# Performance work log

Hardware: AMD Instinct MI355X
Metric: run time of the kernel (lower is better)

The kernel has to match this reference:

```python
import jax, jax.numpy as jnp
import numpy as np

B = 8
N_ANCHORS = 262144
PROPOSAL_COUNT = 1000
IOU_THRESHOLD = 0.7
SOFT_NMS = True
PERFORMANCE_COUNT = 5000
MEAN = np.array([0.0, 0.0, 0.0, 0.0], np.float32)
STD = np.array([0.1, 0.1, 0.2, 0.2], np.float32)
CLIP_RATIO = 16.0 / 1000.0
SOFT_NMS_SIGMA = 0.5  # tf.image.non_max_suppression_with_scores default used by pad_nms
NEG = jnp.float32(-1e9)


def setup_inputs() -> dict:
    key = jax.random.key(0)
    k1, k2, k3, k4, k5 = jax.random.split(key, 5)
    rpn_score = jax.random.uniform(k1, (B, N_ANCHORS, 1), jnp.float32)  # sigmoid-like objectness
    rpn_regress = jax.random.normal(k2, (B, N_ANCHORS, 4), jnp.float32)
    # anchors in normalized x1,y1,x2,y2; centers in [0,1], sizes in [0.02,0.3] (a few fall outside -> exercises valid path)
    cx = jax.random.uniform(k3, (N_ANCHORS,), jnp.float32)
    cy = jax.random.uniform(k4, (N_ANCHORS,), jnp.float32)
    wh = jax.random.uniform(k5, (N_ANCHORS, 2), jnp.float32, minval=0.02, maxval=0.3)
    anchors = jnp.stack([cx - wh[:, 0] * 0.5, cy - wh[:, 1] * 0.5,
                         cx + wh[:, 0] * 0.5, cy + wh[:, 1] * 0.5], axis=-1)
    return {"rpn_score": rpn_score, "rpn_regress": rpn_regress, "anchors": anchors}


def delta2bbox(anchors, deltas):
    # standard mmdet-style decode: denormalize deltas, clip dw/dh, shift/scale anchor box
    d = deltas * jnp.asarray(STD) + jnp.asarray(MEAN)
    max_ratio = abs(float(np.log(CLIP_RATIO)))
    dxy = d[..., :2]
    dwh = jnp.clip(d[..., 2:], -max_ratio, max_ratio)
    awh = anchors[..., 2:] - anchors[..., :2]          # anchor w,h
    actr = (anchors[..., 2:] + anchors[..., :2]) * 0.5  # anchor cx,cy
    ctr = actr + dxy * awh
    wh = awh * jnp.exp(dwh)
    return jnp.concatenate([ctr - wh * 0.5, ctr + wh * 0.5], axis=-1)  # x1,y1,x2,y2


def nms_single(boxes, scores):
    # greedy (soft-)NMS on [P,4] boxes / [P] scores, emitting PROPOSAL_COUNT boxes (zero-padded).
    # IoU is coordinate-order agnostic, so we stay in x1y1x2y2 (TF code round-trips through y1x1y2x2).
    area = (boxes[:, 2] - boxes[:, 0]) * (boxes[:, 3] - boxes[:, 1])

    def step(scores_c, _):
        i = jnp.argmax(scores_c)
        s = scores_c[i]
        b = boxes[i]
        lt = jnp.maximum(b[:2], boxes[:, :2])
        rb = jnp.minimum(b[2:], boxes[:, 2:])
        inter = jnp.prod(jnp.clip(rb - lt, 0.0, None), axis=-1)
        iou = inter / (area[i] + area - inter + 1e-12)
        if SOFT_NMS:
            new_scores = scores_c * jnp.exp(-0.5 * iou * iou / SOFT_NMS_SIGMA)
        else:
            new_scores = jnp.where(iou > IOU_THRESHOLD, NEG, scores_c)
        new_scores = new_scores.at[i].set(NEG)
        sel = jnp.where(s > NEG * 0.5, b, jnp.zeros_like(b))  # zero-pad once candidates exhausted
        return new_scores, sel

    _, out = jax.lax.scan(step, scores, None, length=PROPOSAL_COUNT)
    return out  # [PROPOSAL_COUNT, 4]


def reference(rpn_score, rpn_regress, anchors):
    score = jnp.squeeze(rpn_score, axis=-1)  # [B, A]
    # valid-anchor filtering: TF gathers valid indices (dynamic shape); equivalently mask scores so
    # invalid anchors never survive top-k (num_valid >> performance_count here).
    valid = ((anchors[:, 2] <= 1) & (anchors[:, 3] <= 1) &
             (anchors[:, 0] >= 0) & (anchors[:, 1] >= 0))
    score = jnp.where(valid[None, :], score, -1.0)

    proposals = delta2bbox(anchors[None], rpn_regress)  # [B, A, 4]

    top_scores, top_idx = jax.lax.top_k(score, PERFORMANCE_COUNT)         # [B, P]
    proposals = jnp.take_along_axis(proposals, top_idx[..., None], axis=1)  # [B, P, 4]
    proposals = jnp.clip(proposals, 0.0, 1.0)

    proposals = jax.vmap(nms_single)(proposals, top_scores)  # [B, PROPOSAL_COUNT, 4] (x1,y1,x2,y2)
    return jax.lax.stop_gradient(proposals)
```

## Files before the change

### kernel.cpp

```cpp
#include <hip/hip_runtime.h>
#include <stdint.h>

#pragma clang fp contract(off)

#define N_ANCH 262144
#define BATCH 8
#define TOPK 5000
#define PROP 1000
#define SORTN 8192
#define NEGF -1000000000.0f
#define MAXR 4.135166556742356f
#define NMS_T 512
#define HBINS 256

__device__ __forceinline__ unsigned ord32(float f){
  unsigned u = __float_as_uint(f);
  return (u & 0x80000000u) ? ~u : (u | 0x80000000u);
}
__device__ __forceinline__ float unord32(unsigned o){
  unsigned u = (o & 0x80000000u) ? (o & 0x7FFFFFFFu) : ~o;
  return __uint_as_float(u);
}

__device__ __forceinline__ float masked_score(const float* __restrict__ score,
                                              const float4* __restrict__ anchors,
                                              int b, int i){
  float4 a = anchors[i];
  bool valid = (a.z <= 1.0f) && (a.w <= 1.0f) && (a.x >= 0.0f) && (a.y >= 0.0f);
  float s = score[(size_t)b*N_ANCH + i];
  return valid ? s : -1.0f;
}

__global__ void k_hist1(const float* __restrict__ score, const float4* __restrict__ anchors,
                        unsigned* __restrict__ hist){
  __shared__ unsigned lh[HBINS];
  int b = blockIdx.y; int t = threadIdx.x;
  lh[t] = 0; __syncthreads();
  int base = blockIdx.x * 8192;
  for (int r = 0; r < 32; ++r){
    int i = base + r*256 + t;
    float s = masked_score(score, anchors, b, i);
    unsigned o = ord32(s);
    if (o >= 0xBF000000u){
      int bin = (int)(o >> 16) - 0xBF00;
      atomicAdd(&lh[bin], 1u);
    }
  }
  __syncthreads();
  unsigned v = lh[t];
  if (v) atomicAdd(&hist[(size_t)b*HBINS + t], v);
}

__global__ void k_find1(const unsigned* __restrict__ hist, unsigned* __restrict__ meta){
  int b = blockIdx.x; int t = threadIdx.x;
  __shared__ unsigned part[HBINS];
  part[t] = hist[(size_t)b*HBINS + t];
  __syncthreads();
  if (t == 0){
    unsigned cum = 0; int bsel = 0;
    for (int bin = 128; bin >= 0; --bin){
      cum += part[bin];
      if (cum >= TOPK){ bsel = bin; break; }
    }
    meta[b*8+2] = ((unsigned)(0xBF00 + bsel)) << 16;
  }
}

__global__ void k_compact(const float* __restrict__ score, const float4* __restrict__ anchors,
                          unsigned* __restrict__ meta, unsigned long long* __restrict__ cand){
  int b = blockIdx.y;
  int i = blockIdx.x*blockDim.x + threadIdx.x;
  float s = masked_score(score, anchors, b, i);
  unsigned o = ord32(s);
  unsigned T = meta[b*8+2];
  if (o >= T){
    unsigned pos = atomicAdd(&meta[b*8+3], 1u);
    if (pos < SORTN) cand[(size_t)b*SORTN + pos] = (((unsigned long long)(~o)) << 32) | (unsigned)i;
  }
}

__global__ void __launch_bounds__(1024) k_sort(const unsigned* __restrict__ meta,
                       const unsigned long long* __restrict__ cand,
                       unsigned long long* __restrict__ sorted){
  __shared__ unsigned long long keys[SORTN];
  int b = blockIdx.x; int t = threadIdx.x;
  unsigned cnt = meta[b*8+3];
  if (cnt > (unsigned)SORTN) cnt = SORTN;
  for (unsigned j = t; j < SORTN; j += 1024u)
    keys[j] = (j < cnt) ? cand[(size_t)b*SORTN + j] : ~0ull;
  __syncthreads();
  for (unsigned k = 2; k <= SORTN; k <<= 1){
    for (unsigned j = k>>1; j > 0; j >>= 1){
      for (unsigned i = t; i < SORTN; i += 1024u){
        unsigned l = i ^ j;
        if (l > i){
          unsigned long long a = keys[i], c = keys[l];
          bool up = ((i & k) == 0u);
          if ((a > c) == up){ keys[i] = c; keys[l] = a; }
        }
      }
      __syncthreads();
    }
  }
  for (unsigned j = t; j < TOPK; j += 1024u) sorted[(size_t)b*TOPK + j] = keys[j];
}

#define NMS_UPD(J, S_) do{                                                   \
  int j_ = (J);                                                              \
  if (it > 0){                                                               \
    if (j_ == prevBest){                                                     \
      S_ = NEGF;                                                             \
    } else {                                                                 \
      float4 B_ = bx4[j_];                                                   \
      float ltx_ = fmaxf(bbx, B_.x);                                         \
      float lty_ = fmaxf(bby, B_.y);                                         \
      float rbx_ = fminf(bbz, B_.z);                                         \
      float rby_ = fminf(bbw, B_.w);                                         \
      float iw_ = fmaxf(rbx_-ltx_, 0.f);                                     \
      float ih_ = fmaxf(rby_-lty_, 0.f);                                     \
      float inter_ = iw_*ih_;                                                \
      float aj_ = (B_.z-B_.x)*(B_.w-B_.y);                                   \
      float iou_ = inter_/(ba + aj_ - inter_ + 1e-12f);                      \
      S_ = S_*expf(-(iou_*iou_));                                            \
    }                                                                        \
  }                                                                          \
  if (S_ > bs){ bs = S_; bp = j_; }                                          \
}while(0)

__global__ void __launch_bounds__(NMS_T) k_nms(const unsigned long long* __restrict__ sorted,
                      const float4* __restrict__ anchors, const float4* __restrict__ regress,
                      float* __restrict__ out){
  __shared__ float4 bx4[TOPK];
  __shared__ float  scin[TOPK];
  __shared__ unsigned long long pk[8];
  int b = blockIdx.x; int t = threadIdx.x;
  for (int j = t; j < TOPK; j += NMS_T){
    unsigned long long key = sorted[(size_t)b*TOPK + j];
    unsigned o = ~(unsigned)(key>>32);
    unsigned idx = (unsigned)key;
    float s = unord32(o);
    float4 a = anchors[idx];
    float4 d = regress[(size_t)b*N_ANCH + idx];
    float dx = d.x*0.1f, dy = d.y*0.1f;
    float dw = d.z*0.2f, dh = d.w*0.2f;
    dw = fminf(fmaxf(dw, -MAXR), MAXR);
    dh = fminf(fmaxf(dh, -MAXR), MAXR);
    float aw = a.z - a.x, ah = a.w - a.y;
    float cx = (a.z + a.x)*0.5f, cy = (a.w + a.y)*0.5f;
    float ncx = cx + dx*aw, ncy = cy + dy*ah;
    float nw = aw*expf(dw), nh = ah*expf(dh);
    float x1 = ncx - nw*0.5f, y1 = ncy - nh*0.5f;
    float x2 = ncx + nw*0.5f, y2 = ncy + nh*0.5f;
    x1 = fminf(fmaxf(x1,0.f),1.f); y1 = fminf(fmaxf(y1,0.f),1.f);
    x2 = fminf(fmaxf(x2,0.f),1.f); y2 = fminf(fmaxf(y2,0.f),1.f);
    bx4[j] = make_float4(x1,y1,x2,y2);
    scin[j] = s;
  }
  __syncthreads();
  float S0 = scin[t + 0*NMS_T];
  float S1 = scin[t + 1*NMS_T];
  float S2 = scin[t + 2*NMS_T];
  float S3 = scin[t + 3*NMS_T];
  float S4 = scin[t + 4*NMS_T];
  float S5 = scin[t + 5*NMS_T];
  float S6 = scin[t + 6*NMS_T];
  float S7 = scin[t + 7*NMS_T];
  float S8 = scin[t + 8*NMS_T];
  float S9 = (t + 9*NMS_T < TOPK) ? scin[t + 9*NMS_T] : -INFINITY;
  int lane = t & 63, wid = t >> 6;
  int prevBest = -1;
  float bbx = 0.f, bby = 0.f, bbz = 0.f, bbw = 0.f;
  float ba = 0.f;
  for (int it = 0; it < PROP; ++it){
    float bs = -INFINITY; int bp = 0;
    NMS_UPD(t + 0*NMS_T, S0);
    NMS_UPD(t + 1*NMS_T, S1);
    NMS_UPD(t + 2*NMS_T, S2);
    NMS_UPD(t + 3*NMS_T, S3);
    NMS_UPD(t + 4*NMS_T, S4);
    NMS_UPD(t + 5*NMS_T, S5);
    NMS_UPD(t + 6*NMS_T, S6);
    NMS_UPD(t + 7*NMS_T, S7);
    NMS_UPD(t + 8*NMS_T, S8);
    if (t + 9*NMS_T < TOPK) NMS_UPD(t + 9*NMS_T, S9);
    unsigned long long key = (((unsigned long long)ord32(bs))<<32) | (unsigned)(0xFFFFFFFFu - (unsigned)bp);
    #pragma unroll
    for (int m = 1; m < 64; m <<= 1){
      unsigned long long k2 = __shfl_xor(key, m);
      if (k2 > key) key = k2;
    }
    if (lane == 0) pk[wid] = key;
    __syncthreads();
    #pragma unroll
    for (int w = 0; w < 8; ++w){
      unsigned long long k2 = pk[w];
      if (k2 > key) key = k2;
    }
    int p = (int)(0xFFFFFFFFu - (unsigned)key);
    prevBest = p;
    float4 bbv = bx4[p];
    bbx = bbv.x; bby = bbv.y; bbz = bbv.z; bbw = bbv.w;
    ba = (bbz-bbx)*(bbw-bby);
    if (t == 0){
      float s = unord32((unsigned)(key>>32));
      float4 ob = (s > NEGF*0.5f) ? bbv : make_float4(0.f,0.f,0.f,0.f);
      *(float4*)(out + ((size_t)b*PROP + it)*4) = ob;
    }
    __syncthreads();
  }
}

extern "C" void kernel_launch(void* const* d_in, const int* in_sizes, int n_in,
                              void* d_out, int out_size, void* d_ws, size_t ws_size,
                              hipStream_t stream){
  const float*  score   = (const float*) d_in[0];
  const float4* regress = (const float4*)d_in[1];
  const float4* anchors = (const float4*)d_in[2];
  float* out = (float*)d_out;
  char* ws = (char*)d_ws;
  unsigned* hist = (unsigned*)(ws + 0);
  unsigned* meta = (unsigned*)(ws + 8192);
  unsigned long long* cand   = (unsigned long long*)(ws + 16384);
  unsigned long long* sorted = (unsigned long long*)(ws + 16384 + 524288);

  hipMemsetAsync(ws, 0, 16384, stream);
  dim3 gh(N_ANCH/8192, BATCH);
  k_hist1<<<gh, 256, 0, stream>>>(score, anchors, hist);
  k_find1<<<BATCH, HBINS, 0, stream>>>(hist, meta);
  dim3 gc(N_ANCH/256, BATCH);
  k_compact<<<gc, 256, 0, stream>>>(score, anchors, meta, cand);
  k_sort<<<BATCH, 1024, 0, stream>>>(meta, cand, sorted);
  k_nms<<<BATCH, NMS_T, 0, stream>>>(sorted, anchors, regress, out);
}
```

Measured before the change: 3.172 ms.

## Keep NMS boxes in registers and double-buffer reduction slots to drop a barrier

Each thread now keeps its ten candidate boxes, areas and scores in registers, so the per-iteration IoU loop no longer reads boxes from LDS. Precomputed areas also remove the per-iteration area computation. The per-wave partial maxima are double-buffered by iteration parity, which removes the second __syncthreads in each of the 1000 serial NMS iterations. The cost is higher register pressure with 512 threads per block, and correctness now depends on the parity buffering to avoid a read-after-write race.

```diff
diff --git a/kernel.cpp b/kernel.cpp
--- a/kernel.cpp
+++ b/kernel.cpp
@@ -11,6 +11,7 @@
 #define NEGF -1000000000.0f
 #define MAXR 4.135166556742356f
 #define NMS_T 512
+#define NMS_K 10
 #define HBINS 256
 
 __device__ __forceinline__ unsigned ord32(float f){
@@ -105,108 +106,98 @@
   for (unsigned j = t; j < TOPK; j += 1024u) sorted[(size_t)b*TOPK + j] = keys[j];
 }
 
-#define NMS_UPD(J, S_) do{                                                   \
-  int j_ = (J);                                                              \
-  if (it > 0){                                                               \
-    if (j_ == prevBest){                                                     \
-      S_ = NEGF;                                                             \
-    } else {                                                                 \
-      float4 B_ = bx4[j_];                                                   \
-      float ltx_ = fmaxf(bbx, B_.x);                                         \
-      float lty_ = fmaxf(bby, B_.y);                                         \
-      float rbx_ = fminf(bbz, B_.z);                                         \
-      float rby_ = fminf(bbw, B_.w);                                         \
-      float iw_ = fmaxf(rbx_-ltx_, 0.f);                                     \
-      float ih_ = fmaxf(rby_-lty_, 0.f);                                     \
-      float inter_ = iw_*ih_;                                                \
-      float aj_ = (B_.z-B_.x)*(B_.w-B_.y);                                   \
-      float iou_ = inter_/(ba + aj_ - inter_ + 1e-12f);                      \
-      S_ = S_*expf(-(iou_*iou_));                                            \
-    }                                                                        \
-  }                                                                          \
-  if (S_ > bs){ bs = S_; bp = j_; }                                          \
-}while(0)
-
 __global__ void __launch_bounds__(NMS_T) k_nms(const unsigned long long* __restrict__ sorted,
                       const float4* __restrict__ anchors, const float4* __restrict__ regress,
                       float* __restrict__ out){
   __shared__ float4 bx4[TOPK];
-  __shared__ float  scin[TOPK];
-  __shared__ unsigned long long pk[8];
+  __shared__ unsigned long long pk[2][8];
   int b = blockIdx.x; int t = threadIdx.x;
-  for (int j = t; j < TOPK; j += NMS_T){
-    unsigned long long key = sorted[(size_t)b*TOPK + j];
-    unsigned o = ~(unsigned)(key>>32);
-    unsigned idx = (unsigned)key;
-    float s = unord32(o);
-    float4 a = anchors[idx];
-    float4 d = regress[(size_t)b*N_ANCH + idx];
-    float dx = d.x*0.1f, dy = d.y*0.1f;
-    float dw = d.z*0.2f, dh = d.w*0.2f;
-    dw = fminf(fmaxf(dw, -MAXR), MAXR);
-    dh = fminf(fmaxf(dh, -MAXR), MAXR);
-    float aw = a.z - a.x, ah = a.w - a.y;
-    float cx = (a.z + a.x)*0.5f, cy = (a.w + a.y)*0.5f;
-    float ncx = cx + dx*aw, ncy = cy + dy*ah;
-    float nw = aw*expf(dw), nh = ah*expf(dh);
-    float x1 = ncx - nw*0.5f, y1 = ncy - nh*0.5f;
-    float x2 = ncx + nw*0.5f, y2 = ncy + nh*0.5f;
-    x1 = fminf(fmaxf(x1,0.f),1.f); y1 = fminf(fmaxf(y1,0.f),1.f);
-    x2 = fminf(fmaxf(x2,0.f),1.f); y2 = fminf(fmaxf(y2,0.f),1.f);
-    bx4[j] = make_float4(x1,y1,x2,y2);
-    scin[j] = s;
-  }
-  __syncthreads();
-  float S0 = scin[t + 0*NMS_T];
-  float S1 = scin[t + 1*NMS_T];
-  float S2 = scin[t + 2*NMS_T];
-  float S3 = scin[t + 3*NMS_T];
-  float S4 = scin[t + 4*NMS_T];
-  float S5 = scin[t + 5*NMS_T];
-  float S6 = scin[t + 6*NMS_T];
-  float S7 = scin[t + 7*NMS_T];
-  float S8 = scin[t + 8*NMS_T];
-  float S9 = (t + 9*NMS_T < TOPK) ? scin[t + 9*NMS_T] : -INFINITY;
+  float4 bbx[NMS_K]; float sar[NMS_K]; float sco[NMS_K];
+  #pragma unroll
+  for (int k=0;k<NMS_K;++k){
+    int j = t + k*NMS_T;
+    if (j < TOPK){
+      unsigned long long key = sorted[(size_t)b*TOPK + j];
+      unsigned o = ~(unsigned)(key>>32);
+      unsigned idx = (unsigned)key;
+      float s = unord32(o);
+      float4 a = anchors[idx];
+      float4 d = regress[(size_t)b*N_ANCH + idx];
+      float dx = d.x*0.1f, dy = d.y*0.1f;
+      float dw = d.z*0.2f, dh = d.w*0.2f;
+      dw = fminf(fmaxf(dw, -MAXR), MAXR);
+      dh = fminf(fmaxf(dh, -MAXR), MAXR);
+      float aw = a.z - a.x, ah = a.w - a.y;
+      float cx = (a.z + a.x)*0.5f, cy = (a.w + a.y)*0.5f;
+      float ncx = cx + dx*aw, ncy = cy + dy*ah;
+      float nw = aw*expf(dw), nh = ah*expf(dh);
+      float x1 = ncx - nw*0.5f, y1 = ncy - nh*0.5f;
+      float x2 = ncx + nw*0.5f, y2 = ncy + nh*0.5f;
+      x1 = fminf(fmaxf(x1,0.f),1.f); y1 = fminf(fmaxf(y1,0.f),1.f);
+      x2 = fminf(fmaxf(x2,0.f),1.f); y2 = fminf(fmaxf(y2,0.f),1.f);
+      float4 box = make_float4(x1,y1,x2,y2);
+      bbx[k] = box; bx4[j] = box;
+      sar[k] = (x2-x1)*(y2-y1);
+      sco[k] = s;
+    } else {
+      bbx[k] = make_float4(0.f,0.f,0.f,0.f);
+      sar[k] = 0.f;
+      sco[k] = -INFINITY;
+    }
+  }
+  __syncthreads();
   int lane = t & 63, wid = t >> 6;
   int prevBest = -1;
-  float bbx = 0.f, bby = 0.f, bbz = 0.f, bbw = 0.f;
+  float4 bb = make_float4(0.f,0.f,0.f,0.f);
   float ba = 0.f;
-  for (int it = 0; it < PROP; ++it){
+  for (int it=0; it<PROP; ++it){
     float bs = -INFINITY; int bp = 0;
-    NMS_UPD(t + 0*NMS_T, S0);
-    NMS_UPD(t + 1*NMS_T, S1);
-    NMS_UPD(t + 2*NMS_T, S2);
-    NMS_UPD(t + 3*NMS_T, S3);
-    NMS_UPD(t + 4*NMS_T, S4);
-    NMS_UPD(t + 5*NMS_T, S5);
-    NMS_UPD(t + 6*NMS_T, S6);
-    NMS_UPD(t + 7*NMS_T, S7);
-    NMS_UPD(t + 8*NMS_T, S8);
-    if (t + 9*NMS_T < TOPK) NMS_UPD(t + 9*NMS_T, S9);
+    #pragma unroll
+    for (int k=0;k<NMS_K;++k){
+      int j = t + k*NMS_T;
+      bool inb = (k < NMS_K-1) || (j < TOPK);
+      if (inb){
+        if (it > 0){
+          if (j == prevBest){
+            sco[k] = NEGF;
+          } else {
+            float ltx = fmaxf(bb.x, bbx[k].x);
+            float lty = fmaxf(bb.y, bbx[k].y);
+            float rbx = fminf(bb.z, bbx[k].z);
+            float rby = fminf(bb.w, bbx[k].w);
+            float iw = fmaxf(rbx-ltx, 0.f);
+            float ih = fmaxf(rby-lty, 0.f);
+            float inter = iw*ih;
+            float iou = inter/(ba + sar[k] - inter + 1e-12f);
+            sco[k] = sco[k]*expf(-(iou*iou));
+          }
+        }
+        if (sco[k] > bs){ bs = sco[k]; bp = j; }
+      }
+    }
     unsigned long long key = (((unsigned long long)ord32(bs))<<32) | (unsigned)(0xFFFFFFFFu - (unsigned)bp);
     #pragma unroll
-    for (int m = 1; m < 64; m <<= 1){
+    for (int m=1;m<64;m<<=1){
       unsigned long long k2 = __shfl_xor(key, m);
       if (k2 > key) key = k2;
     }
-    if (lane == 0) pk[wid] = key;
+    int buf = it & 1;
+    if (lane==0) pk[buf][wid] = key;
     __syncthreads();
     #pragma unroll
-    for (int w = 0; w < 8; ++w){
-      unsigned long long k2 = pk[w];
+    for (int w=0;w<8;++w){
+      unsigned long long k2 = pk[buf][w];
       if (k2 > key) key = k2;
     }
     int p = (int)(0xFFFFFFFFu - (unsigned)key);
     prevBest = p;
-    float4 bbv = bx4[p];
-    bbx = bbv.x; bby = bbv.y; bbz = bbv.z; bbw = bbv.w;
-    ba = (bbz-bbx)*(bbw-bby);
-    if (t == 0){
+    bb = bx4[p];
+    ba = (bb.z-bb.x)*(bb.w-bb.y);
+    if (t==0){
       float s = unord32((unsigned)(key>>32));
-      float4 ob = (s > NEGF*0.5f) ? bbv : make_float4(0.f,0.f,0.f,0.f);
+      float4 ob = (s > NEGF*0.5f) ? bb : make_float4(0.f,0.f,0.f,0.f);
       *(float4*)(out + ((size_t)b*PROP + it)*4) = ob;
     }
-    __syncthreads();
   }
 }
 
```

New measurement: 2.702 ms. 1.17x faster.
